# Kernel tuning notes

Hardware: AMD Instinct MI355X
Metric: run time of the kernel (lower is better)

Reference implementation:

```python
import jax, jax.numpy as jnp
import numpy as np

HIDDEN = 2048
N_HEADS = 16
N_KV = 8
HEAD_DIM = HIDDEN // N_HEADS  # 128
EPS = 1e-6


def rms_norm(x, w, eps=EPS):
    xf = x.astype(jnp.float32)
    var = jnp.mean(xf * xf, axis=-1, keepdims=True)
    return (w * (xf * jax.lax.rsqrt(var + eps)).astype(x.dtype))


def rotate_half(x):
    x1, x2 = jnp.split(x, 2, axis=-1)
    return jnp.concatenate([-x2, x1], axis=-1)


def setup_inputs() -> dict:
    key = jax.random.key(0)
    ks = jax.random.split(key, 8)
    B, S = 2, 2048
    inp = {
        "hidden_states": jax.random.normal(ks[0], (B, S, HIDDEN), jnp.float32),
        "cos": jax.random.uniform(ks[1], (B, S, HEAD_DIM), jnp.float32, -1.0, 1.0),
        "sin": jax.random.uniform(ks[2], (B, S, HEAD_DIM), jnp.float32, -1.0, 1.0),
        "Wq": jax.random.normal(ks[3], (N_HEADS * HEAD_DIM, HIDDEN), jnp.float32) * 0.02,
        "Wk": jax.random.normal(ks[4], (N_KV * HEAD_DIM, HIDDEN), jnp.float32) * 0.02,
        "Wv": jax.random.normal(ks[5], (N_KV * HEAD_DIM, HIDDEN), jnp.float32) * 0.02,
        "Wo": jax.random.normal(ks[6], (HIDDEN, N_HEADS * HEAD_DIM), jnp.float32) * 0.02,
        "q_norm_w": jnp.ones((HEAD_DIM,), jnp.float32),
        "k_norm_w": jnp.ones((HEAD_DIM,), jnp.float32),
    }
    return inp


def reference(hidden_states, cos, sin, Wq, Wk, Wv, Wo, q_norm_w, k_norm_w):
    B, S, _ = hidden_states.shape
    scale = HEAD_DIM ** -0.5
    n_rep = N_HEADS // N_KV

    q = (hidden_states @ Wq.T).reshape(B, S, N_HEADS, HEAD_DIM)
    k = (hidden_states @ Wk.T).reshape(B, S, N_KV, HEAD_DIM)
    v = (hidden_states @ Wv.T).reshape(B, S, N_KV, HEAD_DIM)

    q = rms_norm(q, q_norm_w)
    k = rms_norm(k, k_norm_w)

    # -> (B, H, S, D)
    q = q.transpose(0, 2, 1, 3)
    k = k.transpose(0, 2, 1, 3)
    v = v.transpose(0, 2, 1, 3)

    c = cos[:, None, :, :]  # (B,1,S,D)
    s = sin[:, None, :, :]
    q = q * c + rotate_half(q) * s
    k = k * c + rotate_half(k) * s

    k = jnp.repeat(k, n_rep, axis=1)
    v = jnp.repeat(v, n_rep, axis=1)

    scores = jnp.einsum("bhqd,bhkd->bhqk", q, k) * scale
    attn = jax.nn.softmax(scores.astype(jnp.float32), axis=-1).astype(hidden_states.dtype)
    out = jnp.einsum("bhqk,bhkd->bhqd", attn, v)
    out = out.transpose(0, 2, 1, 3).reshape(B, S, N_HEADS * HEAD_DIM)
    return out @ Wo.T
```

## Files before the change

### kernel.cpp

```cpp
#include <hip/hip_runtime.h>
#include <cstdint>

#define SEQ 2048
#define BATCH 2
#define TOK 4096
#define HID 2048
#define NH 16
#define NKV 8
#define HD 128
#define QKV_LD 4096

using f16x8 = __attribute__((ext_vector_type(8))) _Float16;
using f32x4 = __attribute__((ext_vector_type(4))) float;

#define MFMA(a, b, c) __builtin_amdgcn_mfma_f32_16x16x32_f16(a, b, c, 0, 0, 0)

__device__ inline void gload16(const void* g, void* l) {
    __builtin_amdgcn_global_load_lds(
        (const __attribute__((address_space(1))) unsigned*)g,
        (__attribute__((address_space(3))) unsigned*)l, 16, 0, 0);
}

__device__ inline float exp2_fast(float x) {
#if __has_builtin(__builtin_amdgcn_exp2f)
    return __builtin_amdgcn_exp2f(x);
#else
    float r;
    asm("v_exp_f32 %0, %1\n\ts_nop 1" : "=v"(r) : "v"(x));
    return r;
#endif
}

__global__ __launch_bounds__(256) void conv_all(
    const float* __restrict__ hidden, const float* __restrict__ Wq,
    const float* __restrict__ Wk, const float* __restrict__ Wv,
    const float* __restrict__ Wo, _Float16* __restrict__ HhG,
    _Float16* __restrict__ WallH, _Float16* __restrict__ WoH)
{
    const int bid = blockIdx.x;
    const float* src;
    _Float16* dst;
    int row;
    if (bid < 4096)      { row = bid;        src = hidden; dst = HhG; }
    else if (bid < 6144) { row = bid - 4096; src = Wq;     dst = WallH; }
    else if (bid < 7168) { row = bid - 6144; src = Wk;     dst = WallH + (size_t)2048 * HID; }
    else if (bid < 8192) { row = bid - 7168; src = Wv;     dst = WallH + (size_t)3072 * HID; }
    else                 { row = bid - 8192; src = Wo;     dst = WoH; }

    const int gch = threadIdx.x;
    const float* s = src + (size_t)row * HID + gch * 8;
    float4 a = *(const float4*)s;
    float4 b = *(const float4*)(s + 4);
    f16x8 v;
    v[0] = (_Float16)a.x; v[1] = (_Float16)a.y;
    v[2] = (_Float16)a.z; v[3] = (_Float16)a.w;
    v[4] = (_Float16)b.x; v[5] = (_Float16)b.y;
    v[6] = (_Float16)b.z; v[7] = (_Float16)b.w;
    *(f16x8*)((char*)dst + (size_t)row * 4096 + gch * 16) = v;
}

__global__ __launch_bounds__(512, 2) void gemm256(
    const _Float16* __restrict__ Ag, const _Float16* __restrict__ Bg,
    float* __restrict__ C, int ldc, int K)
{
    __shared__ char lds[2][4][16384];

    const int tid = threadIdx.x;
    const int wv = tid >> 6, ln = tid & 63;
    const int wm = wv >> 2, wn = wv & 3;
    const int lr = ln & 15, lq = ln >> 4;
    const int bn = blockIdx.x, bm = blockIdx.y;

    f32x4 acc[8][4] = {};

    const size_t arow0 = (size_t)bm * 256;
    const size_t brow0 = (size_t)bn * 256;

    const int g = tid & 7;
    uint32_t offA[2][2], offB[2][2];
#pragma unroll
    for (int i = 0; i < 2; ++i) {
        const int row = (i * 512 + tid) >> 3;
        const uint32_t sw = (uint32_t)((g ^ (row & 7)) << 4);
        offA[0][i] = (uint32_t)((arow0 + row) * 4096) + sw;
        offA[1][i] = (uint32_t)((arow0 + 128 + row) * 4096) + sw;
        offB[0][i] = (uint32_t)((brow0 + row) * 4096) + sw;
        offB[1][i] = (uint32_t)((brow0 + 128 + row) * 4096) + sw;
    }
    const int dst0 = wv * 64 * 16;

    const int swz0 = ((lq ^ (lr & 7)) << 4);
    const int swz1 = (((4 + lq) ^ (lr & 7)) << 4);

#define STAGE_ALL(bufsel, t)                                                   \
    { _Pragma("unroll")                                                        \
      for (int i = 0; i < 2; ++i) {                                            \
        gload16((const char*)Ag + offA[0][i] + (size_t)(t) * 128,              \
                &lds[bufsel][0][i * 8192 + dst0]);                             \
        gload16((const char*)Ag + offA[1][i] + (size_t)(t) * 128,              \
                &lds[bufsel][1][i * 8192 + dst0]);                             \
        gload16((const char*)Bg + offB[0][i] + (size_t)(t) * 128,              \
                &lds[bufsel][2][i * 8192 + dst0]);                             \
        gload16((const char*)Bg + offB[1][i] + (size_t)(t) * 128,              \
                &lds[bufsel][3][i * 8192 + dst0]);                             \
      } }

    STAGE_ALL(0, 0);
    asm volatile("s_waitcnt vmcnt(0)" ::: "memory");
    __builtin_amdgcn_s_barrier();

    const int NT = K / 64;
    for (int t = 0; t < NT; ++t) {
        const int buf = t & 1;
        const char* Ab = &lds[buf][wm][0];
        const char* Bb = &lds[buf][2 + (wn >> 1)][(wn & 1) * 64 * 128];

        f16x8 bfr[4][2];
#pragma unroll
        for (int nj = 0; nj < 4; ++nj) {
            bfr[nj][0] = *(const f16x8*)(Bb + (nj * 16 + lr) * 128 + swz0);
            bfr[nj][1] = *(const f16x8*)(Bb + (nj * 16 + lr) * 128 + swz1);
        }

        if (t + 1 < NT) STAGE_ALL(buf ^ 1, t + 1);

        __builtin_amdgcn_s_setprio(1);
#pragma unroll
        for (int mi = 0; mi < 8; ++mi) {
            f16x8 a0 = *(const f16x8*)(Ab + (mi * 16 + lr) * 128 + swz0);
            f16x8 a1 = *(const f16x8*)(Ab + (mi * 16 + lr) * 128 + swz1);
#pragma unroll
            for (int nj = 0; nj < 4; ++nj) {
                acc[mi][nj] = MFMA(a0, bfr[nj][0], acc[mi][nj]);
                acc[mi][nj] = MFMA(a1, bfr[nj][1], acc[mi][nj]);
            }
        }
        __builtin_amdgcn_s_setprio(0);

        asm volatile("s_waitcnt vmcnt(0)" ::: "memory");
        __builtin_amdgcn_s_barrier();
    }
#undef STAGE_ALL

#pragma unroll
    for (int mi = 0; mi < 8; ++mi)
#pragma unroll
        for (int r = 0; r < 4; ++r) {
            float* rowp = C + (size_t)(arow0 + wm * 128 + mi * 16 + lq * 4 + r) * ldc
                          + brow0 + wn * 64 + lr;
#pragma unroll
            for (int nj = 0; nj < 4; ++nj)
                rowp[nj * 16] = acc[mi][nj][r];
        }
}

__global__ __launch_bounds__(512, 1) void gemm256x128(
    const _Float16* __restrict__ Ag, const _Float16* __restrict__ Bg,
    float* __restrict__ C, int ldc, int K)
{
    __shared__ char lds[2][3][16384];

    const int tid = threadIdx.x;
    const int wv = tid >> 6, ln = tid & 63;
    const int wm = wv >> 1, wn = wv & 1;
    const int lr = ln & 15, lq = ln >> 4;
    const int bn = blockIdx.x, bm = blockIdx.y;

    f32x4 acc[4][4] = {};

    const size_t arow0 = (size_t)bm * 256;
    const size_t brow0 = (size_t)bn * 128;

    const int g = tid & 7;
    uint32_t offA[2][2], offB[2];
#pragma unroll
    for (int i = 0; i < 2; ++i) {
        const int row = (i * 512 + tid) >> 3;
        const uint32_t sw = (uint32_t)((g ^ (row & 7)) << 4);
        offA[0][i] = (uint32_t)((arow0 + row) * 4096) + sw;
        offA[1][i] = (uint32_t)((arow0 + 128 + row) * 4096) + sw;
        offB[i]    = (uint32_t)((brow0 + row) * 4096) + sw;
    }
    const int dst0 = wv * 64 * 16;

    const int swz0 = ((lq ^ (lr & 7)) << 4);
    const int swz1 = (((4 + lq) ^ (lr & 7)) << 4);

#define STAGE_ALL2(bufsel, t)                                                  \
    { _Pragma("unroll")                                                        \
      for (int i = 0; i < 2; ++i) {                                            \
        gload16((const char*)Ag + offA[0][i] + (size_t)(t) * 128,              \
                &lds[bufsel][0][i * 8192 + dst0]);                             \
        gload16((const char*)Ag + offA[1][i] + (size_t)(t) * 128,              \
                &lds[bufsel][1][i * 8192 + dst0]);                             \
        gload16((const char*)Bg + offB[i] + (size_t)(t) * 128,                 \
                &lds[bufsel][2][i * 8192 + dst0]);                             \
      } }

    STAGE_ALL2(0, 0);
    asm volatile("s_waitcnt vmcnt(0)" ::: "memory");
    __builtin_amdgcn_s_barrier();

    const int NT = K / 64;
    for (int t = 0; t < NT; ++t) {
        const int buf = t & 1;
        const char* Ab = &lds[buf][wm >> 1][(wm & 1) * 64 * 128];
        const char* Bb = &lds[buf][2][wn * 64 * 128];

        f16x8 bfr[4][2];
#pragma unroll
        for (int nj = 0; nj < 4; ++nj) {
            bfr[nj][0] = *(const f16x8*)(Bb + (nj * 16 + lr) * 128 + swz0);
            bfr[nj][1] = *(const f16x8*)(Bb + (nj * 16 + lr) * 128 + swz1);
        }

        if (t + 1 < NT) STAGE_ALL2(buf ^ 1, t + 1);

        __builtin_amdgcn_s_setprio(1);
#pragma unroll
        for (int mi = 0; mi < 4; ++mi) {
            f16x8 a0 = *(const f16x8*)(Ab + (mi * 16 + lr) * 128 + swz0);
            f16x8 a1 = *(const f16x8*)(Ab + (mi * 16 + lr) * 128 + swz1);
#pragma unroll
            for (int nj = 0; nj < 4; ++nj) {
                acc[mi][nj] = MFMA(a0, bfr[nj][0], acc[mi][nj]);
                acc[mi][nj] = MFMA(a1, bfr[nj][1], acc[mi][nj]);
            }
        }
        __builtin_amdgcn_s_setprio(0);

        asm volatile("s_waitcnt vmcnt(0)" ::: "memory");
        __builtin_amdgcn_s_barrier();
    }
#undef STAGE_ALL2

#pragma unroll
    for (int mi = 0; mi < 4; ++mi)
#pragma unroll
        for (int r = 0; r < 4; ++r) {
            float* rowp = C + (size_t)(arow0 + wm * 64 + mi * 16 + lq * 4 + r) * ldc
                          + brow0 + wn * 64 + lr;
#pragma unroll
            for (int nj = 0; nj < 4; ++nj)
                rowp[nj * 16] = acc[mi][nj][r];
        }
}

__global__ __launch_bounds__(256) void norm_rope(
    const float* __restrict__ P, const float* __restrict__ cosb,
    const float* __restrict__ sinb, const float* __restrict__ qw,
    const float* __restrict__ kw, _Float16* __restrict__ QhG,
    _Float16* __restrict__ KhG)
{
    const int t    = blockIdx.y;
    const int wave = threadIdx.x >> 6;
    const int lane = threadIdx.x & 63;
    const int hid  = blockIdx.x * 4 + wave;
    const float QS = 0.08838834764831845f * 1.4426950408889634f;

    const float* ptr;
    const float* w;
    if (hid < NH) { ptr = P + (size_t)t * QKV_LD + hid * HD;              w = qw; }
    else          { ptr = P + (size_t)t * QKV_LD + HID + (hid - NH) * HD; w = kw; }

    float x1 = ptr[lane];
    float x2 = ptr[lane + 64];
    float ss = x1 * x1 + x2 * x2;
#pragma unroll
    for (int off = 1; off < 64; off <<= 1) ss += __shfl_xor(ss, off);
    const float r = rsqrtf(ss * (1.f / 128.f) + 1e-6f);
    const float n1 = x1 * r * w[lane];
    const float n2 = x2 * r * w[lane + 64];

    const float* cp = cosb + (size_t)t * HD;
    const float* sp = sinb + (size_t)t * HD;
    const float o1 = n1 * cp[lane]      - n2 * sp[lane];
    const float o2 = n2 * cp[lane + 64] + n1 * sp[lane + 64];

    if (hid < NH) {
        _Float16* qrow = QhG + (size_t)t * HID + hid * HD;
        qrow[lane]      = (_Float16)(o1 * QS);
        qrow[lane + 64] = (_Float16)(o2 * QS);
    } else {
        const int b = t / SEQ, s = t % SEQ, kv = hid - NH;
        char* ph = (char*)KhG + ((size_t)(b * NKV + kv) * SEQ + s) * 256;
        const int s7 = s & 7;
        const int d1 = lane, d2 = lane + 64;
        *(_Float16*)(ph + (((d1 >> 3) ^ s7) << 4) + ((d1 & 7) << 1)) = (_Float16)o1;
        *(_Float16*)(ph + (((d2 >> 3) ^ s7) << 4) + ((d2 & 7) << 1)) = (_Float16)o2;
    }
}

__global__ __launch_bounds__(256) void conv_v(
    const float* __restrict__ P, _Float16* __restrict__ VtG)
{
    __shared__ float Ts[64][133];
    const int kb = blockIdx.x;
    const int kv = blockIdx.y;
    const int tid = threadIdx.x;

#pragma unroll
    for (int r = 0; r < 8; ++r) {
        const int idx = tid + r * 256;
        const int row = idx >> 5, c4 = (idx & 31) * 4;
        float4 v = *(const float4*)(P + (size_t)(kb * 64 + row) * QKV_LD
                                    + HID + NKV * HD + kv * HD + c4);
        Ts[row][c4 + 0] = v.x; Ts[row][c4 + 1] = v.y;
        Ts[row][c4 + 2] = v.z; Ts[row][c4 + 3] = v.w;
    }
    __syncthreads();

    const int b  = (kb * 64) / SEQ;
    const int s0 = (kb * 64) % SEQ;
#pragma unroll
    for (int w = 0; w < 4; ++w) {
        const int idx = tid + w * 256;
        const int d = idx >> 3, c = idx & 7;
        f16x8 pk;
#pragma unroll
        for (int kk = 0; kk < 8; ++kk) pk[kk] = (_Float16)Ts[c * 8 + kk][d];
        char* dst = (char*)VtG + ((size_t)(b * NKV + kv) * 128 + d) * 4096
                    + ((s0 >> 3) + (c ^ (d & 7))) * 16;
        *(f16x8*)dst = pk;
    }
}

__global__ __launch_bounds__(256, 2) void flash_f16(
    const _Float16* __restrict__ QhG, const _Float16* __restrict__ KhG,
    const _Float16* __restrict__ VtG, _Float16* __restrict__ OH)
{
    __shared__ char KhL[2][16384];
    __shared__ char VtL[16384];
    __shared__ _Float16 Pl[4][32][72];

    const int qt = blockIdx.x, h = blockIdx.y, b = blockIdx.z;
    const int hkv = h >> 1;
    const int tid = threadIdx.x, wv = tid >> 6, ln = tid & 63;
    const int lr = ln & 15, lq = ln >> 4;
    const int qbase = qt * 128 + wv * 32;
    const float BIAS = 3.0f * 1.4426950408889634f;

    f16x8 qh[2][4];
#pragma unroll
    for (int mi = 0; mi < 2; ++mi)
#pragma unroll
        for (int kc = 0; kc < 4; ++kc)
            qh[mi][kc] = *(const f16x8*)(QhG
                + (size_t)(b * SEQ + qbase + mi * 16 + lr) * HID
                + h * HD + kc * 32 + lq * 8);

    f32x4 o_[2][8] = {};
    float rs[2][4] = {};

    const size_t krow = (size_t)(b * NKV + hkv) * SEQ;
    const size_t vrow = (size_t)(b * NKV + hkv) * 128;

    const char* kg[4];
    const char* vg[4];
    int dofs[4];
#pragma unroll
    for (int r = 0; r < 4; ++r) {
        const int idx = tid + r * 256;
        kg[r] = (const char*)KhG + (krow + (idx >> 4)) * 256 + (idx & 15) * 16;
        vg[r] = (const char*)VtG + (vrow + (idx >> 3)) * 4096 + (idx & 7) * 16;
        dofs[r] = (r * 256 + wv * 64) * 16;
    }

#define STAGE_K(buf, kt)                                                      \
    { _Pragma("unroll")                                                       \
      for (int r = 0; r < 4; ++r)                                             \
          gload16(kg[r] + (size_t)(kt) * 16384, &KhL[buf][dofs[r]]); }
#define STAGE_V(kt)                                                           \
    { _Pragma("unroll")                                                       \
      for (int r = 0; r < 4; ++r)                                             \
          gload16(vg[r] + (kt) * 128, &VtL[dofs[r]]); }

    STAGE_K(0, 0);
    STAGE_V(0);
    STAGE_K(1, 1);
    __syncthreads();

    const int NT = SEQ / 64;
    for (int kt = 0; kt < NT; ++kt) {
        const int buf = kt & 1;

        f32x4 s[2][4];
        __builtin_amdgcn_s_setprio(1);
#pragma unroll
        for (int nt = 0; nt < 4; ++nt) {
            const int key = nt * 16 + lr;
            f16x8 kh[4];
#pragma unroll
            for (int kc = 0; kc < 4; ++kc)
                kh[kc] = *(f16x8*)(&KhL[buf][key * 256 +
                                   ((((kc * 4 + lq) ^ (lr & 7))) << 4)]);
#pragma unroll
            for (int mi = 0; mi < 2; ++mi) {
                f32x4 sa = {-BIAS, -BIAS, -BIAS, -BIAS};
#pragma unroll
                for (int kc = 0; kc < 4; ++kc)
                    sa = MFMA(qh[mi][kc], kh[kc], sa);
                s[mi][nt] = sa;
            }
        }
        __builtin_amdgcn_s_setprio(0);

#pragma unroll
        for (int mi = 0; mi < 2; ++mi)
#pragma unroll
            for (int nt = 0; nt < 4; ++nt)
#pragma unroll
                for (int r = 0; r < 4; ++r) {
                    const float p = exp2_fast(s[mi][nt][r]);
                    rs[mi][r] += p;
                    Pl[wv][mi * 16 + lq * 4 + r][nt * 16 + lr] = (_Float16)p;
                }
        f16x8 pa[2][2];
#pragma unroll
        for (int mi = 0; mi < 2; ++mi) {
            pa[mi][0] = *(f16x8*)&Pl[wv][mi * 16 + lr][lq * 8];
            pa[mi][1] = *(f16x8*)&Pl[wv][mi * 16 + lr][32 + lq * 8];
        }

        __syncthreads();

        __builtin_amdgcn_s_setprio(1);
#pragma unroll
        for (int nt2 = 0; nt2 < 8; ++nt2) {
            const int d0 = nt2 * 16 + lr;
            f16x8 v0 = *(f16x8*)(&VtL[d0 * 128 + ((lq ^ (d0 & 7)) << 4)]);
            f16x8 v1 = *(f16x8*)(&VtL[d0 * 128 + (((4 + lq) ^ (d0 & 7)) << 4)]);
#pragma unroll
            for (int mi = 0; mi < 2; ++mi) {
                o_[mi][nt2] = MFMA(pa[mi][0], v0, o_[mi][nt2]);
                o_[mi][nt2] = MFMA(pa[mi][1], v1, o_[mi][nt2]);
            }
        }
        __builtin_amdgcn_s_setprio(0);

        __syncthreads();

        if (kt + 1 < NT) STAGE_V(kt + 1);
        if (kt + 2 < NT) STAGE_K(buf, kt + 2);
    }

    float inv[2][4];
#pragma unroll
    for (int mi = 0; mi < 2; ++mi)
#pragma unroll
        for (int r = 0; r < 4; ++r) {
            float v = rs[mi][r];
            v += __shfl_xor(v, 1);
            v += __shfl_xor(v, 2);
            v += __shfl_xor(v, 4);
            v += __shfl_xor(v, 8);
            inv[mi][r] = 1.0f / v;
        }

#pragma unroll
    for (int mi = 0; mi < 2; ++mi)
#pragma unroll
        for (int r = 0; r < 4; ++r) {
            const int R = b * SEQ + qbase + mi * 16 + lq * 4 + r;
            _Float16* rowp = OH + (size_t)R * HID + h * HD + lr;
#pragma unroll
            for (int nt2 = 0; nt2 < 8; ++nt2)
                rowp[nt2 * 16] = (_Float16)(o_[mi][nt2][r] * inv[mi][r]);
        }
#undef STAGE_K
#undef STAGE_V
}

extern "C" void kernel_launch(void* const* d_in, const int* in_sizes, int n_in,
                              void* d_out, int out_size, void* d_ws, size_t ws_size,
                              hipStream_t stream)
{
    (void)in_sizes; (void)n_in; (void)out_size; (void)ws_size;
    const float* hidden = (const float*)d_in[0];
    const float* cosb   = (const float*)d_in[1];
    const float* sinb   = (const float*)d_in[2];
    const float* Wq     = (const float*)d_in[3];
    const float* Wk     = (const float*)d_in[4];
    const float* Wv     = (const float*)d_in[5];
    const float* Wo     = (const float*)d_in[6];
    const float* qw     = (const float*)d_in[7];
    const float* kw     = (const float*)d_in[8];
    float* out = (float*)d_out;

    char* ws = (char*)d_ws;
    const size_t MB = 1ull << 20;
    float*     P     = (float*)(ws);
    _Float16*  attnH = (_Float16*)(ws + 64  * MB);
    _Float16*  HhG   = (_Float16*)(ws + 80  * MB);
    _Float16*  WallH = (_Float16*)(ws + 96  * MB);
    _Float16*  WoH   = (_Float16*)(ws + 112 * MB);
    _Float16*  KhG   = (_Float16*)(ws + 120 * MB);
    _Float16*  VtG   = (_Float16*)(ws + 128 * MB);
    _Float16*  QhG   = (_Float16*)(ws + 136 * MB);

    const dim3 blk(256);
    conv_all<<<10240, blk, 0, stream>>>(hidden, Wq, Wk, Wv, Wo, HhG, WallH, WoH);

    gemm256<<<dim3(16, 16), dim3(512), 0, stream>>>(HhG, WallH, P, QKV_LD, HID);

    norm_rope<<<dim3(6, TOK), blk, 0, stream>>>(P, cosb, sinb, qw, kw, QhG, KhG);
    conv_v<<<dim3(TOK / 64, NKV), blk, 0, stream>>>(P, VtG);

    flash_f16<<<dim3(SEQ / 128, NH, BATCH), blk, 0, stream>>>(QhG, KhG, VtG, attnH);

    gemm256x128<<<dim3(16, 16), dim3(512), 0, stream>>>(attnH, WoH, out, HID, HID);
}
```

Before: 220.7 us.

## Store QKV projection in fp16, swizzle flash block order, relax V-load wait

The QKV GEMM now writes its output as fp16 instead of fp32, and norm_rope and conv_v read fp16. This halves the intermediate write and read traffic and shrinks the workspace. The flash attention kernel remaps block IDs so that neighbouring blocks are spread across heads and batches. It also replaces a full __syncthreads with a partial vmcnt wait plus a barrier, so the next stage's loads can stay in flight. The cost is rounding the pre-norm projections to fp16, and the partial vmcnt count relies on the exact number of outstanding loads.

Result: faster. 215.3 us (-2.4%).

```diff
diff --git a/kernel.cpp b/kernel.cpp
--- a/kernel.cpp
+++ b/kernel.cpp
@@ -59,9 +59,10 @@
     *(f16x8*)((char*)dst + (size_t)row * 4096 + gch * 16) = v;
 }
 
+template<bool HALF_OUT>
 __global__ __launch_bounds__(512, 2) void gemm256(
     const _Float16* __restrict__ Ag, const _Float16* __restrict__ Bg,
-    float* __restrict__ C, int ldc, int K)
+    void* __restrict__ Cv, int ldc, int K)
 {
     __shared__ char lds[2][4][16384];
 
@@ -146,11 +147,20 @@
     for (int mi = 0; mi < 8; ++mi)
 #pragma unroll
         for (int r = 0; r < 4; ++r) {
-            float* rowp = C + (size_t)(arow0 + wm * 128 + mi * 16 + lq * 4 + r) * ldc
-                          + brow0 + wn * 64 + lr;
-#pragma unroll
-            for (int nj = 0; nj < 4; ++nj)
-                rowp[nj * 16] = acc[mi][nj][r];
+            const size_t rowoff =
+                (size_t)(arow0 + wm * 128 + mi * 16 + lq * 4 + r) * ldc
+                + brow0 + wn * 64 + lr;
+            if constexpr (HALF_OUT) {
+                _Float16* rowp = (_Float16*)Cv + rowoff;
+#pragma unroll
+                for (int nj = 0; nj < 4; ++nj)
+                    rowp[nj * 16] = (_Float16)acc[mi][nj][r];
+            } else {
+                float* rowp = (float*)Cv + rowoff;
+#pragma unroll
+                for (int nj = 0; nj < 4; ++nj)
+                    rowp[nj * 16] = acc[mi][nj][r];
+            }
         }
 }
 
@@ -247,7 +257,7 @@
 }
 
 __global__ __launch_bounds__(256) void norm_rope(
-    const float* __restrict__ P, const float* __restrict__ cosb,
+    const _Float16* __restrict__ P, const float* __restrict__ cosb,
     const float* __restrict__ sinb, const float* __restrict__ qw,
     const float* __restrict__ kw, _Float16* __restrict__ QhG,
     _Float16* __restrict__ KhG)
@@ -258,13 +268,13 @@
     const int hid  = blockIdx.x * 4 + wave;
     const float QS = 0.08838834764831845f * 1.4426950408889634f;
 
-    const float* ptr;
+    const _Float16* ptr;
     const float* w;
     if (hid < NH) { ptr = P + (size_t)t * QKV_LD + hid * HD;              w = qw; }
     else          { ptr = P + (size_t)t * QKV_LD + HID + (hid - NH) * HD; w = kw; }
 
-    float x1 = ptr[lane];
-    float x2 = ptr[lane + 64];
+    float x1 = (float)ptr[lane];
+    float x2 = (float)ptr[lane + 64];
     float ss = x1 * x1 + x2 * x2;
 #pragma unroll
     for (int off = 1; off < 64; off <<= 1) ss += __shfl_xor(ss, off);
@@ -292,21 +302,20 @@
 }
 
 __global__ __launch_bounds__(256) void conv_v(
-    const float* __restrict__ P, _Float16* __restrict__ VtG)
-{
-    __shared__ float Ts[64][133];
+    const _Float16* __restrict__ P, _Float16* __restrict__ VtG)
+{
+    __shared__ _Float16 Ts[64][136];
     const int kb = blockIdx.x;
     const int kv = blockIdx.y;
     const int tid = threadIdx.x;
 
 #pragma unroll
-    for (int r = 0; r < 8; ++r) {
+    for (int r = 0; r < 4; ++r) {
         const int idx = tid + r * 256;
-        const int row = idx >> 5, c4 = (idx & 31) * 4;
-        float4 v = *(const float4*)(P + (size_t)(kb * 64 + row) * QKV_LD
-                                    + HID + NKV * HD + kv * HD + c4);
-        Ts[row][c4 + 0] = v.x; Ts[row][c4 + 1] = v.y;
-        Ts[row][c4 + 2] = v.z; Ts[row][c4 + 3] = v.w;
+        const int row = idx >> 4, c8 = idx & 15;
+        *(f16x8*)&Ts[row][c8 * 8] =
+            *(const f16x8*)(P + (size_t)(kb * 64 + row) * QKV_LD
+                            + HID + NKV * HD + kv * HD + c8 * 8);
     }
     __syncthreads();
 
@@ -318,7 +327,7 @@
         const int d = idx >> 3, c = idx & 7;
         f16x8 pk;
 #pragma unroll
-        for (int kk = 0; kk < 8; ++kk) pk[kk] = (_Float16)Ts[c * 8 + kk][d];
+        for (int kk = 0; kk < 8; ++kk) pk[kk] = Ts[c * 8 + kk][d];
         char* dst = (char*)VtG + ((size_t)(b * NKV + kv) * 128 + d) * 4096
                     + ((s0 >> 3) + (c ^ (d & 7))) * 16;
         *(f16x8*)dst = pk;
@@ -333,7 +342,10 @@
     __shared__ char VtL[16384];
     __shared__ _Float16 Pl[4][32][72];
 
-    const int qt = blockIdx.x, h = blockIdx.y, b = blockIdx.z;
+    const int id  = blockIdx.x + 16 * (blockIdx.y + 16 * blockIdx.z);
+    const int swz = (id & 7) * 64 + (id >> 3);
+    const int qt = swz & 15, h = (swz >> 4) & 15, b = swz >> 8;
+
     const int hkv = h >> 1;
     const int tid = threadIdx.x, wv = tid >> 6, ln = tid & 63;
     const int lr = ln & 15, lq = ln >> 4;
@@ -422,7 +434,12 @@
             pa[mi][1] = *(f16x8*)&Pl[wv][mi * 16 + lr][32 + lq * 8];
         }
 
-        __syncthreads();
+        if (kt + 1 < NT) {
+            asm volatile("s_waitcnt vmcnt(4)" ::: "memory");
+        } else {
+            asm volatile("s_waitcnt vmcnt(0)" ::: "memory");
+        }
+        __builtin_amdgcn_s_barrier();
 
         __builtin_amdgcn_s_setprio(1);
 #pragma unroll
@@ -489,22 +506,22 @@
 
     char* ws = (char*)d_ws;
     const size_t MB = 1ull << 20;
-    float*     P     = (float*)(ws);
-    _Float16*  attnH = (_Float16*)(ws + 64  * MB);
-    _Float16*  HhG   = (_Float16*)(ws + 80  * MB);
-    _Float16*  WallH = (_Float16*)(ws + 96  * MB);
-    _Float16*  WoH   = (_Float16*)(ws + 112 * MB);
-    _Float16*  KhG   = (_Float16*)(ws + 120 * MB);
-    _Float16*  VtG   = (_Float16*)(ws + 128 * MB);
-    _Float16*  QhG   = (_Float16*)(ws + 136 * MB);
+    _Float16*  P16   = (_Float16*)(ws);
+    _Float16*  attnH = (_Float16*)(ws + 32  * MB);
+    _Float16*  HhG   = (_Float16*)(ws + 48  * MB);
+    _Float16*  WallH = (_Float16*)(ws + 64  * MB);
+    _Float16*  WoH   = (_Float16*)(ws + 80  * MB);
+    _Float16*  KhG   = (_Float16*)(ws + 88  * MB);
+    _Float16*  VtG   = (_Float16*)(ws + 96  * MB);
+    _Float16*  QhG   = (_Float16*)(ws + 104 * MB);
 
     const dim3 blk(256);
     conv_all<<<10240, blk, 0, stream>>>(hidden, Wq, Wk, Wv, Wo, HhG, WallH, WoH);
 
-    gemm256<<<dim3(16, 16), dim3(512), 0, stream>>>(HhG, WallH, P, QKV_LD, HID);
-
-    norm_rope<<<dim3(6, TOK), blk, 0, stream>>>(P, cosb, sinb, qw, kw, QhG, KhG);
-    conv_v<<<dim3(TOK / 64, NKV), blk, 0, stream>>>(P, VtG);
+    gemm256<true><<<dim3(16, 16), dim3(512), 0, stream>>>(HhG, WallH, P16, QKV_LD, HID);
+
+    norm_rope<<<dim3(6, TOK), blk, 0, stream>>>(P16, cosb, sinb, qw, kw, QhG, KhG);
+    conv_v<<<dim3(TOK / 64, NKV), blk, 0, stream>>>(P16, VtG);
 
     flash_f16<<<dim3(SEQ / 128, NH, BATCH), blk, 0, stream>>>(QhG, KhG, VtG, attnH);
 
```
